# Kernel tuning notes

Measured on AMD Instinct MI355X. Metric: run time of the kernel, lower is better.

## Reference

```python
import jax, jax.numpy as jnp
import numpy as np

EPS = 1e-5
NUM_HEADS = 16


def _rmsnorm(x, w, eps=EPS):
    var = jnp.mean(jnp.square(x), axis=-1, keepdims=True)
    return x * jax.lax.rsqrt(var + eps) * w


def setup_inputs() -> dict:
    key = jax.random.key(0)
    ks = jax.random.split(key, 7)
    B, T, H = 4, 8192, 1024
    KD, VD = 512, 1024          # key_dim = 0.5*H, value_dim = H
    hk, hv = KD // NUM_HEADS, VD // NUM_HEADS  # 32, 64
    return {
        "hidden_states": jax.random.normal(ks[0], (B, T, H), jnp.float32),
        "recurrent_state": jax.random.normal(ks[1], (B, NUM_HEADS, hk, hv), jnp.float32),
        "norm_w": jax.random.uniform(ks[2], (H,), jnp.float32, 0.5, 1.5),
        "q_w": jax.random.normal(ks[3], (KD, H), jnp.float32) * 0.02,
        "v_norm_w": jax.random.uniform(ks[4], (hv,), jnp.float32, 0.5, 1.5),
        "o_w": jax.random.normal(ks[5], (H, VD), jnp.float32) * 0.02,
        "gate_w": jax.random.normal(ks[6], (H, H), jnp.float32) * 0.02,
    }


def reference(hidden_states, recurrent_state, norm_w, q_w, v_norm_w, o_w, gate_w):
    B, T, H = hidden_states.shape
    nh = NUM_HEADS
    x = _rmsnorm(hidden_states, norm_w)                      # [B,T,H]
    q = (x @ q_w.T).reshape(B, T, nh, -1)                    # [B,T,h,dk]
    # F.normalize(dim=-1): divide by max(L2 norm, 1e-12)
    q = q / jnp.maximum(jnp.linalg.norm(q, axis=-1, keepdims=True), 1e-12)
    o = jnp.einsum('bthk,bhkv->bthv', q, recurrent_state)    # [B,T,h,dv]
    o = _rmsnorm(o, v_norm_w)
    o = o.reshape(B, T, -1) @ o_w.T                          # [B,T,H]
    gate = jax.nn.sigmoid(x @ gate_w.T)                      # [B,T,H]
    return gate * o
```

## Files before the change

### kernel.cpp

```cpp
#include <hip/hip_runtime.h>
#include <hip/hip_bf16.h>
#include <stdint.h>

typedef __attribute__((ext_vector_type(8))) short short8;
typedef __attribute__((ext_vector_type(4))) float floatx4;
typedef __attribute__((ext_vector_type(2))) unsigned int uint2v;

#define DEV static __device__ __forceinline__

DEV unsigned short f2bs(float f) {
  union { float f; unsigned u; } v; v.f = f;
  unsigned u = v.u;
  u += 0x7fffu + ((u >> 16) & 1u);
  return (unsigned short)(u >> 16);
}
DEV float bs2f(unsigned short s) {
  union { unsigned u; float f; } v; v.u = ((unsigned)s) << 16;
  return v.f;
}
DEV unsigned pack2(float a, float b) {
  return (unsigned)f2bs(a) | ((unsigned)f2bs(b) << 16);
}

DEV void gload_lds16(const void* g, void* l) {
  __builtin_amdgcn_global_load_lds(
      (const __attribute__((address_space(1))) void*)g,
      (__attribute__((address_space(3))) void*)l, 16, 0, 0);
}

static constexpr int Hdim = 1024;
static constexpr int KDim = 512;
static constexpr int NH = 16;
static constexpr int HK = 32;
static constexpr int HV = 64;
static constexpr int Mtok = 4 * 8192;

__global__ __launch_bounds__(256) void k_cvt(const float4* __restrict__ in,
                                             uint2v* __restrict__ out, int n4) {
  int i = blockIdx.x * 256 + threadIdx.x;
  if (i >= n4) return;
  float4 v = in[i];
  uint2v o;
  o.x = pack2(v.x, v.y);
  o.y = pack2(v.z, v.w);
  out[i] = o;
}

__global__ __launch_bounds__(256) void k_cvts(const float* __restrict__ S,
                                              unsigned short* __restrict__ St) {
  int i = blockIdx.x * 256 + threadIdx.x;
  if (i >= 4 * NH * HV * HK) return;
  int k = i & 31, v = (i >> 5) & 63, bh = i >> 11;
  St[i] = f2bs(S[(size_t)(bh * HK + k) * HV + v]);
}

__global__ __launch_bounds__(256) void k_rmsnorm(const float* __restrict__ hs,
                                                 const float* __restrict__ nw,
                                                 uint2v* __restrict__ X) {
  const int token = blockIdx.x;
  const int tid = threadIdx.x;
  float4 h = ((const float4*)(hs + (size_t)token * Hdim))[tid];
  float ss = h.x * h.x + h.y * h.y + h.z * h.z + h.w * h.w;
#pragma unroll
  for (int off = 32; off > 0; off >>= 1) ss += __shfl_down(ss, off, 64);
  __shared__ float red[4];
  const int lane = tid & 63, wid = tid >> 6;
  if (lane == 0) red[wid] = ss;
  __syncthreads();
  float tot = red[0] + red[1] + red[2] + red[3];
  float sc = rsqrtf(tot * (1.0f / Hdim) + 1e-5f);
  float4 w = ((const float4*)nw)[tid];
  uint2v o;
  o.x = pack2(h.x * sc * w.x, h.y * sc * w.y);
  o.y = pack2(h.z * sc * w.z, h.w * sc * w.w);
  X[(size_t)token * 256 + tid] = o;
}

DEV void gemm128d(const unsigned short* __restrict__ A,
                  const unsigned short* __restrict__ Bw, const int K,
                  const int m0, const int n0, unsigned short* LDS,
                  floatx4 (&acc)[4][4], const int tid) {
  const int lane = tid & 63;
  const int w = tid >> 6;
  const int wr = w >> 1, wc = w & 1;
  const int frr = lane & 15;
  const int frk = (lane >> 4) * 8;
  const int aswz = (frr & 7) * 8;
  const int r_a = tid >> 3;
  const int c_src = ((tid & 7) ^ (r_a & 7)) * 8;
  const unsigned short* Ag = A + (size_t)(m0 + r_a) * K + c_src;
  const unsigned short* Bg = Bw + (size_t)(n0 + r_a) * K + c_src;
  const int NT = K >> 6;

  {
    char* AsD = (char*)LDS + tid * 16;
    char* BsD = (char*)(LDS + 16384) + tid * 16;
#pragma unroll
    for (int i = 0; i < 4; ++i) {
      gload_lds16(Ag + (size_t)i * 32 * K, AsD + i * 4096);
      gload_lds16(Bg + (size_t)i * 32 * K, BsD + i * 4096);
    }
  }
  asm volatile("s_waitcnt vmcnt(0)" ::: "memory");
  __builtin_amdgcn_s_barrier();
  asm volatile("" ::: "memory");

  int cur = 0;
  for (int t = 0; t < NT; ++t) {
    if (t + 1 < NT) {
      char* AsD = (char*)(LDS + (cur ^ 1) * 8192) + tid * 16;
      char* BsD = (char*)(LDS + 16384 + (cur ^ 1) * 8192) + tid * 16;
      const int k0 = (t + 1) * 64;
#pragma unroll
      for (int i = 0; i < 4; ++i) {
        gload_lds16(Ag + (size_t)i * 32 * K + k0, AsD + i * 4096);
        gload_lds16(Bg + (size_t)i * 32 * K + k0, BsD + i * 4096);
      }
    }
    const unsigned short* Asb = LDS + cur * 8192;
    const unsigned short* Bsb = LDS + 16384 + cur * 8192;
#pragma unroll
    for (int kk = 0; kk < 2; ++kk) {
      short8 a[4], b[4];
#pragma unroll
      for (int mi = 0; mi < 4; ++mi)
        a[mi] = *(const short8*)
            &Asb[(wr * 64 + mi * 16 + frr) * 64 + ((kk * 32 + frk) ^ aswz)];
#pragma unroll
      for (int ni = 0; ni < 4; ++ni)
        b[ni] = *(const short8*)
            &Bsb[(wc * 64 + ni * 16 + frr) * 64 + ((kk * 32 + frk) ^ aswz)];
#pragma unroll
      for (int mi = 0; mi < 4; ++mi)
#pragma unroll
        for (int ni = 0; ni < 4; ++ni)
          acc[mi][ni] = __builtin_amdgcn_mfma_f32_16x16x32_bf16(
              a[mi], b[ni], acc[mi][ni], 0, 0, 0);
    }
    if (t + 1 < NT) {
      asm volatile("s_waitcnt vmcnt(0)" ::: "memory");
      __builtin_amdgcn_s_barrier();
      asm volatile("" ::: "memory");
    }
    cur ^= 1;
  }
  __syncthreads();
}

__global__ __launch_bounds__(256, 2) void k_fused_go(
    const unsigned short* __restrict__ X, const unsigned short* __restrict__ Ob,
    const unsigned short* __restrict__ gwb,
    const unsigned short* __restrict__ owb, float* __restrict__ out) {
  __shared__ unsigned short LDS[4 * 128 * 64];
  const int tid = threadIdx.x;
  const int lane = tid & 63;
  const int w = tid >> 6;
  const int wr = w >> 1, wc = w & 1;
  const int bid = blockIdx.x;
  const int v = (bid & 7) * 256 + (bid >> 3);
  const int m0 = (v >> 3) * 128;
  const int n0 = (v & 7) * 128;

  floatx4 acc[4][4];
#pragma unroll
  for (int i = 0; i < 4; ++i)
#pragma unroll
    for (int j = 0; j < 4; ++j) acc[i][j] = (floatx4){0.f, 0.f, 0.f, 0.f};

  gemm128d(X, gwb, Hdim, m0, n0, LDS, acc, tid);

  unsigned pg[4][4][2];
#pragma unroll
  for (int mi = 0; mi < 4; ++mi)
#pragma unroll
    for (int ni = 0; ni < 4; ++ni) {
      float s0 = 1.0f / (1.0f + __expf(-acc[mi][ni][0]));
      float s1 = 1.0f / (1.0f + __expf(-acc[mi][ni][1]));
      float s2 = 1.0f / (1.0f + __expf(-acc[mi][ni][2]));
      float s3 = 1.0f / (1.0f + __expf(-acc[mi][ni][3]));
      pg[mi][ni][0] = pack2(s0, s1);
      pg[mi][ni][1] = pack2(s2, s3);
      acc[mi][ni] = (floatx4){0.f, 0.f, 0.f, 0.f};
    }

  gemm128d(Ob, owb, Hdim, m0, n0, LDS, acc, tid);

  const int rb = (lane >> 4) * 4;
#pragma unroll
  for (int mi = 0; mi < 4; ++mi)
#pragma unroll
    for (int ni = 0; ni < 4; ++ni) {
      const int n = n0 + wc * 64 + ni * 16 + (lane & 15);
#pragma unroll
      for (int r = 0; r < 4; ++r) {
        const int m = m0 + wr * 64 + mi * 16 + rb + r;
        float g = bs2f((unsigned short)(pg[mi][ni][r >> 1] >> ((r & 1) * 16)));
        out[(size_t)m * Hdim + n] = g * acc[mi][ni][r];
      }
    }
}

__global__ __launch_bounds__(256, 2) void k_fused_q(
    const unsigned short* __restrict__ X, const unsigned short* __restrict__ qwb,
    const unsigned short* __restrict__ St, const float* __restrict__ vnw,
    unsigned short* __restrict__ Ob) {
  __shared__ unsigned short LD[4 * 128 * 64];
  const int tid = threadIdx.x;
  const int lane = tid & 63;
  const int w = tid >> 6;
  const int wr = w >> 1, wc = w & 1;
  const int bid = blockIdx.x;
  const int v = (bid & 7) * 128 + (bid >> 3);
  const int m0 = (v >> 2) * 128;
  const int n0 = (v & 3) * 128;
  const int h0 = n0 >> 5;
  const int batch = m0 >> 13;

  floatx4 acc[4][4];
#pragma unroll
  for (int i = 0; i < 4; ++i)
#pragma unroll
    for (int j = 0; j < 4; ++j) acc[i][j] = (floatx4){0.f, 0.f, 0.f, 0.f};

  gemm128d(X, qwb, Hdim, m0, n0, LD, acc, tid);

  const int rb = (lane >> 4) * 4;
  const int frr = lane & 15;
#pragma unroll
  for (int mi = 0; mi < 4; ++mi)
#pragma unroll
    for (int p = 0; p < 2; ++p) {
#pragma unroll
      for (int r = 0; r < 4; ++r) {
        float v0 = acc[mi][2 * p][r], v1 = acc[mi][2 * p + 1][r];
        float ss = v0 * v0 + v1 * v1;
        ss += __shfl_xor(ss, 1, 64);
        ss += __shfl_xor(ss, 2, 64);
        ss += __shfl_xor(ss, 4, 64);
        ss += __shfl_xor(ss, 8, 64);
        const float inv = 1.0f / fmaxf(sqrtf(ss), 1e-12f);
        const int m = wr * 64 + mi * 16 + rb + r;
        const int c0 = wc * 64 + p * 32 + frr;
        const int sw = (m & 7) * 8;
        LD[m * 128 + (c0 ^ sw)] = f2bs(v0 * inv);
        LD[m * 128 + ((c0 + 16) ^ sw)] = f2bs(v1 * inv);
      }
    }
  __syncthreads();

  const int frk = (lane >> 4) * 8;
  float wv[4];
#pragma unroll
  for (int ni = 0; ni < 4; ++ni) wv[ni] = vnw[ni * 16 + frr];

#pragma unroll
  for (int hh = 0; hh < 4; ++hh) {
    const unsigned short* Sp =
        St + (size_t)(batch * NH + h0 + hh) * (HV * HK);
    short8 bfr[4];
#pragma unroll
    for (int ni = 0; ni < 4; ++ni)
      bfr[ni] = *(const short8*)&Sp[(ni * 16 + frr) * HK + frk];
    floatx4 acc2[2][4];
#pragma unroll
    for (int i = 0; i < 2; ++i)
#pragma unroll
      for (int j = 0; j < 4; ++j) acc2[i][j] = (floatx4){0.f, 0.f, 0.f, 0.f};
    short8 af[2];
#pragma unroll
    for (int mi2 = 0; mi2 < 2; ++mi2) {
      const int m = w * 32 + mi2 * 16 + frr;
      af[mi2] = *(const short8*)&LD[m * 128 + ((hh * 32 + frk) ^ ((m & 7) * 8))];
    }
#pragma unroll
    for (int mi2 = 0; mi2 < 2; ++mi2)
#pragma unroll
      for (int ni = 0; ni < 4; ++ni)
        acc2[mi2][ni] = __builtin_amdgcn_mfma_f32_16x16x32_bf16(
            af[mi2], bfr[ni], acc2[mi2][ni], 0, 0, 0);

#pragma unroll
    for (int mi2 = 0; mi2 < 2; ++mi2)
#pragma unroll
      for (int r = 0; r < 4; ++r) {
        float ss2 = 0.f;
#pragma unroll
        for (int ni = 0; ni < 4; ++ni) ss2 += acc2[mi2][ni][r] * acc2[mi2][ni][r];
        ss2 += __shfl_xor(ss2, 1, 64);
        ss2 += __shfl_xor(ss2, 2, 64);
        ss2 += __shfl_xor(ss2, 4, 64);
        ss2 += __shfl_xor(ss2, 8, 64);
        const float sc = rsqrtf(ss2 * (1.0f / HV) + 1e-5f);
        const int m = m0 + w * 32 + mi2 * 16 + rb + r;
        unsigned short* Op = Ob + (size_t)m * Hdim + (h0 + hh) * HV;
#pragma unroll
        for (int ni = 0; ni < 4; ++ni)
          Op[ni * 16 + frr] = f2bs(acc2[mi2][ni][r] * sc * wv[ni]);
      }
  }
}

extern "C" void kernel_launch(void* const* d_in, const int* in_sizes, int n_in,
                              void* d_out, int out_size, void* d_ws, size_t ws_size,
                              hipStream_t stream) {
  const float* hs = (const float*)d_in[0];
  const float* Srec = (const float*)d_in[1];
  const float* nw = (const float*)d_in[2];
  const float* qw = (const float*)d_in[3];
  const float* vnw = (const float*)d_in[4];
  const float* ow = (const float*)d_in[5];
  const float* gw = (const float*)d_in[6];

  char* ws = (char*)d_ws;
  unsigned short* X = (unsigned short*)(ws);
  unsigned short* Ob = (unsigned short*)(ws + ((size_t)64 << 20));
  unsigned short* qwb = (unsigned short*)(ws + ((size_t)128 << 20));
  unsigned short* gwb = (unsigned short*)(ws + ((size_t)129 << 20));
  unsigned short* owb = (unsigned short*)(ws + ((size_t)131 << 20));
  unsigned short* Stb = (unsigned short*)(ws + ((size_t)133 << 20));

  k_cvt<<<(KDim * Hdim / 4 + 255) / 256, 256, 0, stream>>>(
      (const float4*)qw, (uint2v*)qwb, KDim * Hdim / 4);
  k_cvt<<<(Hdim * Hdim / 4 + 255) / 256, 256, 0, stream>>>(
      (const float4*)gw, (uint2v*)gwb, Hdim * Hdim / 4);
  k_cvt<<<(Hdim * Hdim / 4 + 255) / 256, 256, 0, stream>>>(
      (const float4*)ow, (uint2v*)owb, Hdim * Hdim / 4);
  k_cvts<<<(4 * NH * HV * HK + 255) / 256, 256, 0, stream>>>(Srec, Stb);

  k_rmsnorm<<<Mtok, 256, 0, stream>>>(hs, nw, (uint2v*)X);

  k_fused_q<<<(Mtok / 128) * (KDim / 128), 256, 0, stream>>>(
      X, qwb, Stb, vnw, Ob);

  k_fused_go<<<(Mtok / 128) * (Hdim / 128), 256, 0, stream>>>(
      X, Ob, gwb, owb, (float*)d_out);
}
```

Baseline: 262.7 us.

## Split fused gate/output GEMM into two 256x256 pipelined GEMM kernels

Replaces the fused 128x128 gate+output GEMM kernel with a new 512-thread, 256x256-tile GEMM kernel that interleaves staged half-tile loads with four MFMA phases using barriers and s_setprio. The gate GEMM now writes bf16 sigmoid outputs to a workspace buffer, and the output GEMM reads it back in its epilogue. The aim is better operand reuse per tile and overlap of global-to-LDS loads with MFMA work. In exchange it adds an extra 64 MB round trip of the gate tensor through memory and a much more complex synchronization schedule.

```diff
diff --git a/kernel.cpp b/kernel.cpp
--- a/kernel.cpp
+++ b/kernel.cpp
@@ -7,6 +7,7 @@
 typedef __attribute__((ext_vector_type(2))) unsigned int uint2v;
 
 #define DEV static __device__ __forceinline__
+#define FENCE() asm volatile("" ::: "memory")
 
 DEV unsigned short f2bs(float f) {
   union { float f; unsigned u; } v; v.f = f;
@@ -74,6 +75,184 @@
   o.x = pack2(h.x * sc * w.x, h.y * sc * w.y);
   o.y = pack2(h.z * sc * w.z, h.w * sc * w.w);
   X[(size_t)token * 256 + tid] = o;
+}
+
+DEV void stage_half(const unsigned short* __restrict__ G, int ldg,
+                    unsigned short* lds, int tid) {
+  const int r = tid >> 3;
+  const int c = ((tid & 7) ^ (r & 7)) * 8;
+  const unsigned short* src = G + (size_t)r * ldg + c;
+  char* dst = (char*)lds + tid * 16;
+  gload_lds16(src, dst);
+  gload_lds16(src + (size_t)64 * ldg, dst + 8192);
+}
+
+template <int EPI>
+__global__ __launch_bounds__(512, 2) void k_gemm256p(
+    const unsigned short* __restrict__ A, const unsigned short* __restrict__ Bw,
+    void* __restrict__ Cout, const unsigned short* __restrict__ Gate,
+    const int N, const int K) {
+  __shared__ unsigned short LDS[2][4][128 * 64];
+  const int tid = threadIdx.x;
+  const int lane = tid & 63;
+  const int w = tid >> 6;
+  const int wr = w >> 2, wc = w & 3;
+  const int wcH = wc >> 1;
+  const int rB0 = (wc & 1) * 64;
+
+  const int nwg = gridDim.x;
+  const int bid = blockIdx.x;
+  const int cpx = nwg >> 3;
+  const int v = (bid & 7) * cpx + (bid >> 3);
+  const int ncols = N >> 8;
+  const int row = v / ncols, col = v % ncols;
+  const int m0 = row << 8, n0 = col << 8;
+
+  floatx4 acc[8][4];
+#pragma unroll
+  for (int i = 0; i < 8; ++i)
+#pragma unroll
+    for (int j = 0; j < 4; ++j) acc[i][j] = (floatx4){0.f, 0.f, 0.f, 0.f};
+
+  const unsigned short* Ab = A + (size_t)m0 * K;
+  const unsigned short* Bb = Bw + (size_t)n0 * K;
+  const int frr = lane & 15;
+  const int frk = (lane >> 4) * 8;
+  const int swz = (frr & 7) * 8;
+  const int NT = K >> 6;
+
+  stage_half(Ab, K, LDS[0][0], tid);
+  stage_half(Ab + (size_t)128 * K, K, LDS[0][1], tid);
+  stage_half(Bb, K, LDS[0][2], tid);
+  stage_half(Bb + (size_t)128 * K, K, LDS[0][3], tid);
+  stage_half(Bb + 64, K, LDS[1][2], tid);
+  stage_half(Bb + (size_t)128 * K + 64, K, LDS[1][3], tid);
+  asm volatile("s_waitcnt vmcnt(4)" ::: "memory");
+  __builtin_amdgcn_s_barrier();
+  FENCE();
+
+  for (int t = 0; t < NT; ++t) {
+    const unsigned short* Ah = LDS[t & 1][wr];
+    const unsigned short* Bh = LDS[t & 1][2 + wcH];
+    short8 afl[2][4], afh[2][4], bf01[2][2], bf23[2][2];
+
+#pragma unroll
+    for (int kh = 0; kh < 2; ++kh)
+#pragma unroll
+      for (int mi = 0; mi < 4; ++mi)
+        afl[kh][mi] = *(const short8*)
+            &Ah[(mi * 16 + frr) * 64 + ((kh * 32 + frk) ^ swz)];
+#pragma unroll
+    for (int kh = 0; kh < 2; ++kh)
+#pragma unroll
+      for (int ni = 0; ni < 2; ++ni)
+        bf01[kh][ni] = *(const short8*)
+            &Bh[(rB0 + ni * 16 + frr) * 64 + ((kh * 32 + frk) ^ swz)];
+    if (t + 1 < NT)
+      stage_half(Ab + (size_t)(t + 1) * 64, K, LDS[(t + 1) & 1][0], tid);
+    FENCE();
+    __builtin_amdgcn_s_barrier();
+    asm volatile("s_waitcnt lgkmcnt(0)" ::: "memory");
+    __builtin_amdgcn_s_setprio(1);
+#pragma unroll
+    for (int kh = 0; kh < 2; ++kh)
+#pragma unroll
+      for (int mi = 0; mi < 4; ++mi)
+#pragma unroll
+        for (int ni = 0; ni < 2; ++ni)
+          acc[mi][ni] = __builtin_amdgcn_mfma_f32_16x16x32_bf16(
+              afl[kh][mi], bf01[kh][ni], acc[mi][ni], 0, 0, 0);
+    __builtin_amdgcn_s_setprio(0);
+    __builtin_amdgcn_s_barrier();
+
+#pragma unroll
+    for (int kh = 0; kh < 2; ++kh)
+#pragma unroll
+      for (int ni = 0; ni < 2; ++ni)
+        bf23[kh][ni] = *(const short8*)
+            &Bh[(rB0 + (ni + 2) * 16 + frr) * 64 + ((kh * 32 + frk) ^ swz)];
+    if (t + 1 < NT)
+      stage_half(Ab + (size_t)128 * K + (t + 1) * 64, K, LDS[(t + 1) & 1][1],
+                 tid);
+    FENCE();
+    __builtin_amdgcn_s_barrier();
+    asm volatile("s_waitcnt lgkmcnt(0)" ::: "memory");
+    __builtin_amdgcn_s_setprio(1);
+#pragma unroll
+    for (int kh = 0; kh < 2; ++kh)
+#pragma unroll
+      for (int mi = 0; mi < 4; ++mi)
+#pragma unroll
+        for (int ni = 0; ni < 2; ++ni)
+          acc[mi][ni + 2] = __builtin_amdgcn_mfma_f32_16x16x32_bf16(
+              afl[kh][mi], bf23[kh][ni], acc[mi][ni + 2], 0, 0, 0);
+    __builtin_amdgcn_s_setprio(0);
+    __builtin_amdgcn_s_barrier();
+
+#pragma unroll
+    for (int kh = 0; kh < 2; ++kh)
+#pragma unroll
+      for (int mi = 0; mi < 4; ++mi)
+        afh[kh][mi] = *(const short8*)
+            &Ah[((mi + 4) * 16 + frr) * 64 + ((kh * 32 + frk) ^ swz)];
+    if (t + 2 < NT)
+      stage_half(Bb + (size_t)(t + 2) * 64, K, LDS[t & 1][2], tid);
+    FENCE();
+    __builtin_amdgcn_s_barrier();
+    asm volatile("s_waitcnt lgkmcnt(0)" ::: "memory");
+    __builtin_amdgcn_s_setprio(1);
+#pragma unroll
+    for (int kh = 0; kh < 2; ++kh)
+#pragma unroll
+      for (int mi = 0; mi < 4; ++mi)
+#pragma unroll
+        for (int ni = 0; ni < 2; ++ni)
+          acc[mi + 4][ni + 2] = __builtin_amdgcn_mfma_f32_16x16x32_bf16(
+              afh[kh][mi], bf23[kh][ni], acc[mi + 4][ni + 2], 0, 0, 0);
+    __builtin_amdgcn_s_setprio(0);
+    __builtin_amdgcn_s_barrier();
+
+    if (t + 2 < NT) {
+      stage_half(Bb + (size_t)128 * K + (t + 2) * 64, K, LDS[t & 1][3], tid);
+      asm volatile("s_waitcnt vmcnt(4)" ::: "memory");
+    } else {
+      asm volatile("s_waitcnt vmcnt(0)" ::: "memory");
+    }
+    __builtin_amdgcn_s_barrier();
+    __builtin_amdgcn_s_setprio(1);
+#pragma unroll
+    for (int kh = 0; kh < 2; ++kh)
+#pragma unroll
+      for (int mi = 0; mi < 4; ++mi)
+#pragma unroll
+        for (int ni = 0; ni < 2; ++ni)
+          acc[mi + 4][ni] = __builtin_amdgcn_mfma_f32_16x16x32_bf16(
+              afh[kh][mi], bf01[kh][ni], acc[mi + 4][ni], 0, 0, 0);
+    __builtin_amdgcn_s_setprio(0);
+    __builtin_amdgcn_s_barrier();
+    FENCE();
+  }
+
+  const int rb = (lane >> 4) * 4;
+#pragma unroll
+  for (int mi = 0; mi < 8; ++mi)
+#pragma unroll
+    for (int ni = 0; ni < 4; ++ni) {
+      const floatx4 vv = acc[mi][ni];
+      const int n = n0 + wc * 64 + ni * 16 + frr;
+#pragma unroll
+      for (int r = 0; r < 4; ++r) {
+        const int m = m0 + wr * 128 + mi * 16 + rb + r;
+        const size_t idx = (size_t)m * N + n;
+        if (EPI == 1) {
+          float s = 1.0f / (1.0f + __expf(-vv[r]));
+          ((unsigned short*)Cout)[idx] = f2bs(s);
+        } else {
+          float g = bs2f(Gate[idx]);
+          ((float*)Cout)[idx] = g * vv[r];
+        }
+      }
+    }
 }
 
 DEV void gemm128d(const unsigned short* __restrict__ A,
@@ -103,7 +282,7 @@
   }
   asm volatile("s_waitcnt vmcnt(0)" ::: "memory");
   __builtin_amdgcn_s_barrier();
-  asm volatile("" ::: "memory");
+  FENCE();
 
   int cur = 0;
   for (int t = 0; t < NT; ++t) {
@@ -140,64 +319,11 @@
     if (t + 1 < NT) {
       asm volatile("s_waitcnt vmcnt(0)" ::: "memory");
       __builtin_amdgcn_s_barrier();
-      asm volatile("" ::: "memory");
+      FENCE();
     }
     cur ^= 1;
   }
   __syncthreads();
-}
-
-__global__ __launch_bounds__(256, 2) void k_fused_go(
-    const unsigned short* __restrict__ X, const unsigned short* __restrict__ Ob,
-    const unsigned short* __restrict__ gwb,
-    const unsigned short* __restrict__ owb, float* __restrict__ out) {
-  __shared__ unsigned short LDS[4 * 128 * 64];
-  const int tid = threadIdx.x;
-  const int lane = tid & 63;
-  const int w = tid >> 6;
-  const int wr = w >> 1, wc = w & 1;
-  const int bid = blockIdx.x;
-  const int v = (bid & 7) * 256 + (bid >> 3);
-  const int m0 = (v >> 3) * 128;
-  const int n0 = (v & 7) * 128;
-
-  floatx4 acc[4][4];
-#pragma unroll
-  for (int i = 0; i < 4; ++i)
-#pragma unroll
-    for (int j = 0; j < 4; ++j) acc[i][j] = (floatx4){0.f, 0.f, 0.f, 0.f};
-
-  gemm128d(X, gwb, Hdim, m0, n0, LDS, acc, tid);
-
-  unsigned pg[4][4][2];
-#pragma unroll
-  for (int mi = 0; mi < 4; ++mi)
-#pragma unroll
-    for (int ni = 0; ni < 4; ++ni) {
-      float s0 = 1.0f / (1.0f + __expf(-acc[mi][ni][0]));
-      float s1 = 1.0f / (1.0f + __expf(-acc[mi][ni][1]));
-      float s2 = 1.0f / (1.0f + __expf(-acc[mi][ni][2]));
-      float s3 = 1.0f / (1.0f + __expf(-acc[mi][ni][3]));
-      pg[mi][ni][0] = pack2(s0, s1);
-      pg[mi][ni][1] = pack2(s2, s3);
-      acc[mi][ni] = (floatx4){0.f, 0.f, 0.f, 0.f};
-    }
-
-  gemm128d(Ob, owb, Hdim, m0, n0, LDS, acc, tid);
-
-  const int rb = (lane >> 4) * 4;
-#pragma unroll
-  for (int mi = 0; mi < 4; ++mi)
-#pragma unroll
-    for (int ni = 0; ni < 4; ++ni) {
-      const int n = n0 + wc * 64 + ni * 16 + (lane & 15);
-#pragma unroll
-      for (int r = 0; r < 4; ++r) {
-        const int m = m0 + wr * 64 + mi * 16 + rb + r;
-        float g = bs2f((unsigned short)(pg[mi][ni][r >> 1] >> ((r & 1) * 16)));
-        out[(size_t)m * Hdim + n] = g * acc[mi][ni][r];
-      }
-    }
 }
 
 __global__ __launch_bounds__(256, 2) void k_fused_q(
@@ -255,8 +381,7 @@
 
 #pragma unroll
   for (int hh = 0; hh < 4; ++hh) {
-    const unsigned short* Sp =
-        St + (size_t)(batch * NH + h0 + hh) * (HV * HK);
+    const unsigned short* Sp = St + (size_t)(batch * NH + h0 + hh) * (HV * HK);
     short8 bfr[4];
 #pragma unroll
     for (int ni = 0; ni < 4; ++ni)
@@ -314,10 +439,11 @@
   char* ws = (char*)d_ws;
   unsigned short* X = (unsigned short*)(ws);
   unsigned short* Ob = (unsigned short*)(ws + ((size_t)64 << 20));
-  unsigned short* qwb = (unsigned short*)(ws + ((size_t)128 << 20));
-  unsigned short* gwb = (unsigned short*)(ws + ((size_t)129 << 20));
-  unsigned short* owb = (unsigned short*)(ws + ((size_t)131 << 20));
-  unsigned short* Stb = (unsigned short*)(ws + ((size_t)133 << 20));
+  unsigned short* Gs = (unsigned short*)(ws + ((size_t)128 << 20));
+  unsigned short* qwb = (unsigned short*)(ws + ((size_t)192 << 20));
+  unsigned short* gwb = (unsigned short*)(ws + ((size_t)193 << 20));
+  unsigned short* owb = (unsigned short*)(ws + ((size_t)195 << 20));
+  unsigned short* Stb = (unsigned short*)(ws + ((size_t)197 << 20));
 
   k_cvt<<<(KDim * Hdim / 4 + 255) / 256, 256, 0, stream>>>(
       (const float4*)qw, (uint2v*)qwb, KDim * Hdim / 4);
@@ -332,6 +458,9 @@
   k_fused_q<<<(Mtok / 128) * (KDim / 128), 256, 0, stream>>>(
       X, qwb, Stb, vnw, Ob);
 
-  k_fused_go<<<(Mtok / 128) * (Hdim / 128), 256, 0, stream>>>(
-      X, Ob, gwb, owb, (float*)d_out);
-}
+  k_gemm256p<1><<<(Mtok / 256) * (Hdim / 256), 512, 0, stream>>>(
+      X, gwb, Gs, nullptr, Hdim, Hdim);
+
+  k_gemm256p<2><<<(Mtok / 256) * (Hdim / 256), 512, 0, stream>>>(
+      Ob, owb, (float*)d_out, Gs, Hdim, Hdim);
+}
```

Result: slower. 294.8 us (+12.2%).
